# Kernel tuning notes

Measured on AMD Instinct MI355X. Metric: run time of the kernel, lower is better.

Reference implementation:

```python
import jax, jax.numpy as jnp
import numpy as np

N_HEADS = 16


def setup_inputs() -> dict:
    key = jax.random.key(0)
    ks = jax.random.split(key, 5)
    B, S, D = 2, 2048, 1024
    x = jax.random.normal(ks[0], (B, S, D), dtype=jnp.float32)
    Wqkv = jax.random.normal(ks[1], (D, 3 * D), dtype=jnp.float32) * (1.0 / np.sqrt(D))
    bqkv = jax.random.normal(ks[2], (3 * D,), dtype=jnp.float32) * 0.02
    Wout = jax.random.normal(ks[3], (D, D), dtype=jnp.float32) * (1.0 / np.sqrt(D))
    bout = jax.random.normal(ks[4], (D,), dtype=jnp.float32) * 0.02
    return {"x": x, "Wqkv": Wqkv, "bqkv": bqkv, "Wout": Wout, "bout": bout}


def reference(x, Wqkv, bqkv, Wout, bout):
    B, S, D = x.shape
    H = N_HEADS
    dh = D // H
    # qkv projection, then view as [B,S,H,3*dh] and chunk on last dim
    # (matches torch: per-head q/k/v are interleaved slices of the projection)
    qkv = (x @ Wqkv + bqkv).reshape(B, S, H, 3 * dh).transpose(0, 2, 1, 3)  # [B,H,S,3dh]
    q, k, v = jnp.split(qkv, 3, axis=-1)  # each [B,H,S,dh]
    scale = jnp.asarray(1.0 / np.sqrt(dh), dtype=x.dtype)
    scores = jnp.einsum('bhqd,bhkd->bhqk', q, k) * scale  # [B,H,S,S]
    causal = jnp.tril(jnp.ones((S, S), dtype=bool))
    scores = jnp.where(causal, scores, jnp.asarray(-jnp.inf, dtype=scores.dtype))
    attn_w = jax.nn.softmax(scores, axis=-1)
    attn = jnp.einsum('bhqk,bhkd->bhqd', attn_w, v)  # [B,H,S,dh]
    attn = attn.transpose(0, 2, 1, 3).reshape(B, S, D)
    return attn @ Wout + bout
```

## Files before the change

### kernel.cpp

```cpp
#include <hip/hip_runtime.h>
#include <hip/hip_bf16.h>
#include <cstdint>
#include <cstddef>

typedef __hip_bfloat16 bf16;
typedef short bf16x4 __attribute__((ext_vector_type(4)));
typedef short bf16x8 __attribute__((ext_vector_type(8)));
typedef float f32x4 __attribute__((ext_vector_type(4)));

#define LOG2E 1.44269504088896f

static constexpr int Bb = 2, S = 2048, D = 1024, H = 16, DH = 64;

struct TrueT  { static constexpr bool value = true;  };
struct FalseT { static constexpr bool value = false; };

__device__ inline short f2bf_bits(float f) {
  bf16 b = __float2bfloat16(f);
  short s;
  __builtin_memcpy(&s, &b, 2);
  return s;
}
__device__ inline float bfbits2f(short s) {
  uint32_t u = ((uint32_t)(uint16_t)s) << 16;
  float f;
  __builtin_memcpy(&f, &u, 4);
  return f;
}

__global__ __launch_bounds__(256) void prep_kernel(
    const float* __restrict__ Wqkv, bf16* __restrict__ wqkvT,
    const float* __restrict__ Wout, bf16* __restrict__ woutT,
    const float* __restrict__ x, bf16* __restrict__ xbf) {
  const int blk = blockIdx.x;
  const int tid = threadIdx.x;
  if (blk < 4096) {
    __shared__ float t[32][33];
    const float* in;
    bf16* out;
    int R, C, bx, by;
    if (blk < 3072) { in = Wqkv; out = wqkvT; R = 1024; C = 3072; bx = blk % 96; by = blk / 96; }
    else            { in = Wout; out = woutT; R = 1024; C = 1024; bx = (blk - 3072) % 32; by = (blk - 3072) / 32; }
    int c0 = bx * 32, r0 = by * 32;
    int tx = tid & 31, ty = tid >> 5;
#pragma unroll
    for (int i = 0; i < 4; i++) {
      int r = ty + i * 8;
      t[r][tx] = in[(size_t)(r0 + r) * C + c0 + tx];
    }
    __syncthreads();
#pragma unroll
    for (int i = 0; i < 4; i++) {
      int c = ty + i * 8;
      out[(size_t)(c0 + c) * R + r0 + tx] = __float2bfloat16(t[tx][c]);
    }
  } else {
    size_t i = ((size_t)(blk - 4096) * 256 + tid) * 8;
    f32x4 a = *(const f32x4*)(x + i);
    f32x4 b = *(const f32x4*)(x + i + 4);
    bf16x8 v;
#pragma unroll
    for (int j = 0; j < 4; j++) { v[j] = f2bf_bits(a[j]); v[4 + j] = f2bf_bits(b[j]); }
    *(bf16x8*)((short*)xbf + i) = v;
  }
}

__global__ __launch_bounds__(256) void gemm_qkv(
    const bf16* __restrict__ A, const bf16* __restrict__ Bt,
    const float* __restrict__ bias,
    bf16* __restrict__ Qb, bf16* __restrict__ Kb, bf16* __restrict__ Vtb) {
  constexpr int K = 1024;
  __shared__ __align__(16) short smA[128 * 32];
  __shared__ __align__(16) short smB[128 * 32];
  __shared__ __align__(16) short smE[4][16 * 72];

  const int tid = threadIdx.x;
  const int wave = tid >> 6, lane = tid & 63;
  const int quad = lane >> 4, l16 = lane & 15;
  const int m0 = blockIdx.y * 128, n0 = blockIdx.x * 128;
  const int wm = wave >> 1, wn = wave & 1;

  f32x4 acc[4][4];
#pragma unroll
  for (int i = 0; i < 4; i++)
#pragma unroll
    for (int j = 0; j < 4; j++) acc[i][j] = {0.f, 0.f, 0.f, 0.f};

  const int srow = lane >> 2;
  const int scol = (lane & 3) * 8;

  for (int k0 = 0; k0 < K; k0 += 32) {
#pragma unroll
    for (int half = 0; half < 2; half++) {
      int row = half * 64 + wave * 16 + srow;
      const bf16* ga = A + (size_t)(m0 + row) * K + k0 + scol;
      const bf16* gb = Bt + (size_t)(n0 + row) * K + k0 + scol;
      __builtin_amdgcn_global_load_lds(
          (const __attribute__((address_space(1))) void*)ga,
          (__attribute__((address_space(3))) void*)&smA[(half * 64 + wave * 16) * 32],
          16, 0, 0);
      __builtin_amdgcn_global_load_lds(
          (const __attribute__((address_space(1))) void*)gb,
          (__attribute__((address_space(3))) void*)&smB[(half * 64 + wave * 16) * 32],
          16, 0, 0);
    }
    __syncthreads();

    bf16x8 af[4], bf_[4];
#pragma unroll
    for (int mi = 0; mi < 4; mi++)
      af[mi] = *(const bf16x8*)&smA[(wm * 64 + mi * 16 + l16) * 32 + quad * 8];
#pragma unroll
    for (int ni = 0; ni < 4; ni++)
      bf_[ni] = *(const bf16x8*)&smB[(wn * 64 + ni * 16 + l16) * 32 + quad * 8];
#pragma unroll
    for (int mi = 0; mi < 4; mi++)
#pragma unroll
      for (int ni = 0; ni < 4; ni++)
        acc[mi][ni] = __builtin_amdgcn_mfma_f32_16x16x32_bf16(
            af[mi], bf_[ni], acc[mi][ni], 0, 0, 0);
    __syncthreads();
  }

  const int cs0 = n0 + wn * 64;
  const int h = cs0 / 192;
  const int rt = (cs0 >> 6) % 3;
  const int t0w = m0 + wm * 64;
  const int b = t0w >> 11, s0w = t0w & 2047;

  float bv[4];
#pragma unroll
  for (int ni = 0; ni < 4; ni++) bv[ni] = bias[cs0 + ni * 16 + l16];

  if (rt < 2) {
    const float qscale = (rt == 0) ? (0.125f * LOG2E) : 1.0f;
    bf16* dst = (rt == 0 ? Qb : Kb) + ((size_t)(b * H + h) * S + s0w) * 64;
    short* sE = &smE[wave][0];
    const int r8 = lane >> 2, s4 = lane & 3;
#pragma unroll
    for (int mi = 0; mi < 4; mi++) {
#pragma unroll
      for (int ni = 0; ni < 4; ni++)
#pragma unroll
        for (int r = 0; r < 4; r++)
          sE[(quad * 4 + r) * 72 + ni * 16 + l16] =
              f2bf_bits((acc[mi][ni][r] + bv[ni]) * qscale);
      asm volatile("s_waitcnt lgkmcnt(0)" ::: "memory");
      bf16x8 w0 = *(const bf16x8*)&sE[r8 * 72 + s4 * 16];
      bf16x8 w1 = *(const bf16x8*)&sE[r8 * 72 + s4 * 16 + 8];
      short* g = (short*)dst + (size_t)(mi * 16 + r8) * 64 + s4 * 16;
      *(bf16x8*)g = w0;
      *(bf16x8*)(g + 8) = w1;
      asm volatile("s_waitcnt lgkmcnt(0)" ::: "memory");
    }
  } else {
#pragma unroll
    for (int ni = 0; ni < 4; ni++) {
      const int dh = ni * 16 + l16;
#pragma unroll
      for (int mi = 0; mi < 4; mi++) {
        const int s0 = s0w + mi * 16 + quad * 4;
        size_t base = ((size_t)(b * H + h) * 64 + dh) * S + s0;
        bf16x4 vv;
#pragma unroll
        for (int r = 0; r < 4; r++) vv[r] = f2bf_bits(acc[mi][ni][r] + bv[ni]);
        *(bf16x4*)((short*)Vtb + base) = vv;
      }
    }
  }
}

__global__ __launch_bounds__(256) void gemm_out(
    const bf16* __restrict__ A, const bf16* __restrict__ Bt,
    const float* __restrict__ bias, float* __restrict__ C,
    int M, int N, int K) {
  constexpr int BN = 64, NF = 2;
  __shared__ __align__(16) short smA[128 * 32];
  __shared__ __align__(16) short smB[BN * 32];
  __shared__ __align__(16) float smEf[4][580];

  const int tid = threadIdx.x;
  const int wave = tid >> 6, lane = tid & 63;
  const int quad = lane >> 4, l16 = lane & 15;
  const int m0 = blockIdx.y * 128, n0 = blockIdx.x * BN;
  const int wm = wave >> 1, wn = wave & 1;

  f32x4 acc[4][NF];
#pragma unroll
  for (int i = 0; i < 4; i++)
#pragma unroll
    for (int j = 0; j < NF; j++) acc[i][j] = {0.f, 0.f, 0.f, 0.f};

  const int srow = lane >> 2;
  const int scol = (lane & 3) * 8;

  for (int k0 = 0; k0 < K; k0 += 32) {
#pragma unroll
    for (int half = 0; half < 2; half++) {
      int row = half * 64 + wave * 16 + srow;
      const bf16* ga = A + (size_t)(m0 + row) * K + k0 + scol;
      __builtin_amdgcn_global_load_lds(
          (const __attribute__((address_space(1))) void*)ga,
          (__attribute__((address_space(3))) void*)&smA[(half * 64 + wave * 16) * 32],
          16, 0, 0);
    }
    {
      int row = wave * 16 + srow;
      const bf16* gb = Bt + (size_t)(n0 + row) * K + k0 + scol;
      __builtin_amdgcn_global_load_lds(
          (const __attribute__((address_space(1))) void*)gb,
          (__attribute__((address_space(3))) void*)&smB[(wave * 16) * 32],
          16, 0, 0);
    }
    __syncthreads();

    bf16x8 af[4], bf_[NF];
#pragma unroll
    for (int mi = 0; mi < 4; mi++)
      af[mi] = *(const bf16x8*)&smA[(wm * 64 + mi * 16 + l16) * 32 + quad * 8];
#pragma unroll
    for (int ni = 0; ni < NF; ni++)
      bf_[ni] = *(const bf16x8*)&smB[(wn * 32 + ni * 16 + l16) * 32 + quad * 8];
#pragma unroll
    for (int mi = 0; mi < 4; mi++)
#pragma unroll
      for (int ni = 0; ni < NF; ni++)
        acc[mi][ni] = __builtin_amdgcn_mfma_f32_16x16x32_bf16(
            af[mi], bf_[ni], acc[mi][ni], 0, 0, 0);
    __syncthreads();
  }

  float bv[NF];
#pragma unroll
  for (int ni = 0; ni < NF; ni++) bv[ni] = bias[n0 + wn * 32 + ni * 16 + l16];

  float* sE = &smEf[wave][0];
#pragma unroll
  for (int mi = 0; mi < 4; mi++) {
#pragma unroll
    for (int ni = 0; ni < NF; ni++)
#pragma unroll
      for (int r = 0; r < 4; r++)
        sE[(quad * 4 + r) * 36 + ni * 16 + l16] = acc[mi][ni][r] + bv[ni];
    asm volatile("s_waitcnt lgkmcnt(0)" ::: "memory");
#pragma unroll
    for (int t = 0; t < 2; t++) {
      int slot = t * 64 + lane;
      int rr = slot >> 3, c4 = slot & 7;
      f32x4 v = *(const f32x4*)&sE[rr * 36 + c4 * 4];
      int row = m0 + wm * 64 + mi * 16 + rr;
      int col = n0 + wn * 32 + c4 * 4;
      *(f32x4*)&C[(size_t)row * N + col] = v;
    }
    asm volatile("s_waitcnt lgkmcnt(0)" ::: "memory");
  }
}

__global__ __launch_bounds__(256) void attn_kernel(
    const bf16* __restrict__ Qb, const bf16* __restrict__ Kb,
    const bf16* __restrict__ Vtb,
    bf16* __restrict__ Op0, bf16* __restrict__ Op1,
    float* __restrict__ lp0, float* __restrict__ lp1,
    bf16* __restrict__ Ofinal, int split) {
  const int blk = blockIdx.x;
  const int xcd = blk & 7;
  const int idx = blk >> 3;
  int sk, p, bh;
  if (split == 2) { bh = xcd + 8 * (idx / 32); int r = idx % 32; p = r & 15; sk = r >> 4; }
  else            { bh = xcd + 8 * (idx / 16); p = idx & 15; sk = 0; }
  const int h = bh & (H - 1), b = bh >> 4;
  const int tid = threadIdx.x;
  const int wave = tid >> 6, lane = tid & 63;
  const int quad = lane >> 4, l16 = lane & 15;

  bf16*  __restrict__ Op = sk ? Op1 : Op0;
  float* __restrict__ lp = sk ? lp1 : lp0;

  const bf16* Qh = Qb + (size_t)(b * H + h) * S * 64;
  const bf16* Kh = Kb + (size_t)(b * H + h) * S * 64;
  const bf16* Vth = Vtb + (size_t)(b * H + h) * 64 * S;

  __shared__ __align__(16) short smK[2][64 * 64];
  __shared__ __align__(16) short smVt[2][64 * 64];
  __shared__ __align__(16) short pLds[4][16][64];

  const int lrow = lane >> 3;
  const int lg = lane & 7;
  const int swz = l16 & 7;
  const int psw = (l16 & 7) << 1;

  bf16x8 onesB;
#pragma unroll
  for (int j = 0; j < 8; j++) onesB[j] = (short)0x3F80;

  auto stage = [&](int it2, int bufi) {
    const int kv0 = it2 * 64;
#pragma unroll
    for (int j = 0; j < 2; j++) {
      const int row = wave * 16 + j * 8 + lrow;
      const bf16* ks = Kh + (size_t)(kv0 + row) * 64 + (lg ^ (row & 7)) * 8;
      __builtin_amdgcn_global_load_lds(
          (const __attribute__((address_space(1))) void*)ks,
          (__attribute__((address_space(3))) void*)&smK[bufi][(wave * 16 + j * 8) * 64],
          16, 0, 0);
      const bf16* vs = Vth + (size_t)row * S + kv0 + (lg ^ (row & 7)) * 8;
      __builtin_amdgcn_global_load_lds(
          (const __attribute__((address_space(1))) void*)vs,
          (__attribute__((address_space(3))) void*)&smVt[bufi][(wave * 16 + j * 8) * 64],
          16, 0, 0);
    }
  };

#pragma unroll
  for (int pass = 0; pass < 2; pass++) {
    const int qt = pass ? p : (31 - p);
    const int q0 = qt * 64 + wave * 16;
    const int qglob = q0 + l16;

    bf16x8 aQ[2];
#pragma unroll
    for (int kh = 0; kh < 2; kh++)
      aQ[kh] = *(const bf16x8*)(Qh + (size_t)(q0 + l16) * 64 + kh * 32 + quad * 8);

    f32x4 o[4];
#pragma unroll
    for (int dt = 0; dt < 4; dt++) o[dt] = {0.f, 0.f, 0.f, 0.f};
    f32x4 lacc = {0.f, 0.f, 0.f, 0.f};

    auto compute_tile = [&](int it2, int bufi, auto diag_tag) {
      constexpr bool DIAG = decltype(diag_tag)::value;
      const int kv0 = it2 * 64;

      f32x4 z[4];
      __builtin_amdgcn_s_setprio(1);
#pragma unroll
      for (int nh = 0; nh < 4; nh++) {
        const int row = nh * 16 + l16;
        f32x4 t = {0.f, 0.f, 0.f, 0.f};
#pragma unroll
        for (int kh = 0; kh < 2; kh++) {
          bf16x8 bK = *(const bf16x8*)&smK[bufi][row * 64 + ((kh * 4 + quad) ^ swz) * 8];
          t = __builtin_amdgcn_mfma_f32_16x16x32_bf16(bK, aQ[kh], t, 0, 0, 0);
        }
        z[nh] = t;
      }
      __builtin_amdgcn_s_setprio(0);

#pragma unroll
      for (int nh = 0; nh < 4; nh++) {
        bf16x4 pk;
#pragma unroll
        for (int r = 0; r < 4; r++) {
          float e = exp2f(z[nh][r]);
          if (DIAG) {
            const int kidx = kv0 + nh * 16 + quad * 4 + r;
            e = (kidx <= qglob) ? e : 0.f;
          }
          pk[r] = f2bf_bits(e);
        }
        const int gw = (nh * 4 + quad) ^ psw;
        *(bf16x4*)&pLds[wave][l16][gw * 4] = pk;
      }

      asm volatile("s_waitcnt lgkmcnt(0)" ::: "memory");

      bf16x8 aP[2];
#pragma unroll
      for (int k2 = 0; k2 < 2; k2++) {
        const int gr = (k2 * 8 + quad * 2) ^ psw;
        aP[k2] = *(const bf16x8*)&pLds[wave][l16][gr * 4];
      }
      __builtin_amdgcn_s_setprio(1);
#pragma unroll
      for (int k2 = 0; k2 < 2; k2++)
        lacc = __builtin_amdgcn_mfma_f32_16x16x32_bf16(aP[k2], onesB, lacc, 0, 0, 0);
#pragma unroll
      for (int dt = 0; dt < 4; dt++) {
        const int row = dt * 16 + l16;
#pragma unroll
        for (int k2 = 0; k2 < 2; k2++) {
          bf16x8 bV = *(const bf16x8*)&smVt[bufi][row * 64 + ((k2 * 4 + quad) ^ swz) * 8];
          o[dt] = __builtin_amdgcn_mfma_f32_16x16x32_bf16(aP[k2], bV, o[dt], 0, 0, 0);
        }
      }
      __builtin_amdgcn_s_setprio(0);
    };

    int it = sk;
    __syncthreads();
    if (it <= qt) stage(it, 0);
    __syncthreads();
    int cur = 0;
    while (it <= qt) {
      const int next = it + split;
      if (next <= qt) stage(next, cur ^ 1);
      if (it == qt) compute_tile(it, cur, TrueT{});
      else          compute_tile(it, cur, FalseT{});
      __syncthreads();
      cur ^= 1;
      it = next;
    }

    const int rl = lane >> 2, cq = lane & 3;
    short* pw = &pLds[wave][0][0];
    if (split > 1) {
      const size_t rowbase = (size_t)(b * H + h) * S + q0;
      if (l16 == 0) {
#pragma unroll
        for (int r = 0; r < 4; r++) lp[rowbase + quad * 4 + r] = lacc[r];
      }
#pragma unroll
      for (int dt = 0; dt < 4; dt++)
#pragma unroll
        for (int r = 0; r < 4; r++)
          pw[(quad * 4 + r) * 64 + dt * 16 + l16] = f2bf_bits(o[dt][r]);
      asm volatile("s_waitcnt lgkmcnt(0)" ::: "memory");
      bf16x8 w0 = *(const bf16x8*)&pw[rl * 64 + cq * 16];
      bf16x8 w1 = *(const bf16x8*)&pw[rl * 64 + cq * 16 + 8];
      short* g = (short*)Op + (rowbase + rl) * 64 + cq * 16;
      *(bf16x8*)g = w0;
      *(bf16x8*)(g + 8) = w1;
      asm volatile("s_waitcnt lgkmcnt(0)" ::: "memory");
    } else {
      float invr[4];
#pragma unroll
      for (int r = 0; r < 4; r++) invr[r] = 1.f / lacc[r];
#pragma unroll
      for (int dt = 0; dt < 4; dt++)
#pragma unroll
        for (int r = 0; r < 4; r++)
          pw[(quad * 4 + r) * 64 + dt * 16 + l16] = f2bf_bits(o[dt][r] * invr[r]);
      asm volatile("s_waitcnt lgkmcnt(0)" ::: "memory");
      bf16x8 w0 = *(const bf16x8*)&pw[rl * 64 + cq * 16];
      bf16x8 w1 = *(const bf16x8*)&pw[rl * 64 + cq * 16 + 8];
      short* g = (short*)Ofinal + (size_t)(b * S + q0 + rl) * D + h * 64 + cq * 16;
      *(bf16x8*)g = w0;
      *(bf16x8*)(g + 8) = w1;
      asm volatile("s_waitcnt lgkmcnt(0)" ::: "memory");
    }
  }
}

__global__ __launch_bounds__(256) void attn_reduce(
    const bf16* __restrict__ O0, const bf16* __restrict__ O1,
    const float* __restrict__ l0, const float* __restrict__ l1,
    bf16* __restrict__ attnO) {
  int gid = blockIdx.x * 256 + threadIdx.x;
  int row = gid >> 3;
  int c8 = (gid & 7) * 8;
  float inv = 1.f / (l0[row] + l1[row]);
  bf16x8 a = *(const bf16x8*)((const short*)O0 + (size_t)row * 64 + c8);
  bf16x8 bb = *(const bf16x8*)((const short*)O1 + (size_t)row * 64 + c8);
  bf16x8 o;
#pragma unroll
  for (int j = 0; j < 8; j++)
    o[j] = f2bf_bits((bfbits2f(a[j]) + bfbits2f(bb[j])) * inv);
  int bh = row >> 11, q = row & 2047;
  int b = bh >> 4, h = bh & 15;
  *(bf16x8*)((short*)attnO + (((size_t)(b * S + q) * H + h) * 64 + c8)) = o;
}

extern "C" void kernel_launch(void* const* d_in, const int* in_sizes, int n_in,
                              void* d_out, int out_size, void* d_ws, size_t ws_size,
                              hipStream_t stream) {
  const float* x    = (const float*)d_in[0];
  const float* Wqkv = (const float*)d_in[1];
  const float* bqkv = (const float*)d_in[2];
  const float* Wout = (const float*)d_in[3];
  const float* bout = (const float*)d_in[4];
  float* out = (float*)d_out;

  char* ws = (char*)d_ws;
  const bool split2 = (ws_size >= 50855936);

  bf16* Qb  = (bf16*)(ws);
  bf16* Kb  = (bf16*)(ws + 8388608);
  bf16* Vtb = (bf16*)(ws + 16777216);
  bf16* xbf = (bf16*)(ws + 25165824);

  bf16 *Op0 = nullptr, *Op1 = nullptr, *attnO;
  float *lp0 = nullptr, *lp1 = nullptr;
  bf16 *wqkvT, *woutT;
  if (split2) {
    Op0   = (bf16*)(ws + 25165824);
    Op1   = (bf16*)(ws + 33554432);
    lp0   = (float*)(ws + 41943040);
    lp1   = (float*)(ws + 42205184);
    attnO = (bf16*)(ws + 8388608);
    wqkvT = (bf16*)(ws + 42467328);
    woutT = (bf16*)(ws + 48758784);
  } else {
    attnO = (bf16*)(ws + 25165824);
    wqkvT = (bf16*)(ws + 33554432);
    woutT = (bf16*)(ws + 39845888);
  }

  prep_kernel<<<dim3(6144), 256, 0, stream>>>(Wqkv, wqkvT, Wout, woutT, x, xbf);

  gemm_qkv<<<dim3(3072 / 128, 4096 / 128), 256, 0, stream>>>(
      xbf, wqkvT, bqkv, Qb, Kb, Vtb);

  if (split2) {
    attn_kernel<<<dim3(1024), 256, 0, stream>>>(
        Qb, Kb, Vtb, Op0, Op1, lp0, lp1, nullptr, 2);
    attn_reduce<<<dim3(2048), 256, 0, stream>>>(Op0, Op1, lp0, lp1, attnO);
  } else {
    attn_kernel<<<dim3(512), 256, 0, stream>>>(
        Qb, Kb, Vtb, nullptr, nullptr, nullptr, nullptr, attnO, 1);
  }

  gemm_out<<<dim3(1024 / 64, 4096 / 128), 256, 0, stream>>>(
      attnO, woutT, bout, out, 4096, 1024, 1024);
}
```

Measured before the change: 194.7 us.

## Swizzle GEMM LDS tiles, pad attention P buffer, drop split-KV attention path

Both GEMM kernels now XOR-swizzle the 16-byte column chunk on the global-to-LDS load and apply the same swizzle on the MFMA fragment reads, aiming to cut LDS bank conflicts. The attention P/output staging buffer switches from an XOR swizzle to a padded row stride of 76. The two-way KV split and its reduce kernel are removed, so attention always runs 512 blocks and normalizes in place. This saves a kernel launch and the partial-output traffic, but it lowers parallelism for the long causal rows.

Result: faster. 184.1 us (-5.4%).

```diff
diff --git a/kernel.cpp b/kernel.cpp
--- a/kernel.cpp
+++ b/kernel.cpp
@@ -87,7 +87,8 @@
     for (int j = 0; j < 4; j++) acc[i][j] = {0.f, 0.f, 0.f, 0.f};
 
   const int srow = lane >> 2;
-  const int scol = (lane & 3) * 8;
+  const int scol = ((lane & 3) ^ ((lane >> 3) & 3)) * 8;
+  const int gsw = (l16 >> 1) & 3;
 
   for (int k0 = 0; k0 < K; k0 += 32) {
 #pragma unroll
@@ -109,10 +110,10 @@
     bf16x8 af[4], bf_[4];
 #pragma unroll
     for (int mi = 0; mi < 4; mi++)
-      af[mi] = *(const bf16x8*)&smA[(wm * 64 + mi * 16 + l16) * 32 + quad * 8];
+      af[mi] = *(const bf16x8*)&smA[(wm * 64 + mi * 16 + l16) * 32 + (quad ^ gsw) * 8];
 #pragma unroll
     for (int ni = 0; ni < 4; ni++)
-      bf_[ni] = *(const bf16x8*)&smB[(wn * 64 + ni * 16 + l16) * 32 + quad * 8];
+      bf_[ni] = *(const bf16x8*)&smB[(wn * 64 + ni * 16 + l16) * 32 + (quad ^ gsw) * 8];
 #pragma unroll
     for (int mi = 0; mi < 4; mi++)
 #pragma unroll
@@ -192,7 +193,8 @@
     for (int j = 0; j < NF; j++) acc[i][j] = {0.f, 0.f, 0.f, 0.f};
 
   const int srow = lane >> 2;
-  const int scol = (lane & 3) * 8;
+  const int scol = ((lane & 3) ^ ((lane >> 3) & 3)) * 8;
+  const int gsw = (l16 >> 1) & 3;
 
   for (int k0 = 0; k0 < K; k0 += 32) {
 #pragma unroll
@@ -217,10 +219,10 @@
     bf16x8 af[4], bf_[NF];
 #pragma unroll
     for (int mi = 0; mi < 4; mi++)
-      af[mi] = *(const bf16x8*)&smA[(wm * 64 + mi * 16 + l16) * 32 + quad * 8];
+      af[mi] = *(const bf16x8*)&smA[(wm * 64 + mi * 16 + l16) * 32 + (quad ^ gsw) * 8];
 #pragma unroll
     for (int ni = 0; ni < NF; ni++)
-      bf_[ni] = *(const bf16x8*)&smB[(wn * 32 + ni * 16 + l16) * 32 + quad * 8];
+      bf_[ni] = *(const bf16x8*)&smB[(wn * 32 + ni * 16 + l16) * 32 + (quad ^ gsw) * 8];
 #pragma unroll
     for (int mi = 0; mi < 4; mi++)
 #pragma unroll
@@ -258,36 +260,28 @@
 
 __global__ __launch_bounds__(256) void attn_kernel(
     const bf16* __restrict__ Qb, const bf16* __restrict__ Kb,
-    const bf16* __restrict__ Vtb,
-    bf16* __restrict__ Op0, bf16* __restrict__ Op1,
-    float* __restrict__ lp0, float* __restrict__ lp1,
-    bf16* __restrict__ Ofinal, int split) {
+    const bf16* __restrict__ Vtb, bf16* __restrict__ Ofinal) {
   const int blk = blockIdx.x;
   const int xcd = blk & 7;
   const int idx = blk >> 3;
-  int sk, p, bh;
-  if (split == 2) { bh = xcd + 8 * (idx / 32); int r = idx % 32; p = r & 15; sk = r >> 4; }
-  else            { bh = xcd + 8 * (idx / 16); p = idx & 15; sk = 0; }
+  const int bh = xcd + 8 * (idx >> 4);
+  const int p = idx & 15;
   const int h = bh & (H - 1), b = bh >> 4;
   const int tid = threadIdx.x;
   const int wave = tid >> 6, lane = tid & 63;
   const int quad = lane >> 4, l16 = lane & 15;
 
-  bf16*  __restrict__ Op = sk ? Op1 : Op0;
-  float* __restrict__ lp = sk ? lp1 : lp0;
-
   const bf16* Qh = Qb + (size_t)(b * H + h) * S * 64;
   const bf16* Kh = Kb + (size_t)(b * H + h) * S * 64;
   const bf16* Vth = Vtb + (size_t)(b * H + h) * 64 * S;
 
   __shared__ __align__(16) short smK[2][64 * 64];
   __shared__ __align__(16) short smVt[2][64 * 64];
-  __shared__ __align__(16) short pLds[4][16][64];
+  __shared__ __align__(16) short pLds[4][16][76];
 
   const int lrow = lane >> 3;
   const int lg = lane & 7;
   const int swz = l16 & 7;
-  const int psw = (l16 & 7) << 1;
 
   bf16x8 onesB;
 #pragma unroll
@@ -358,18 +352,15 @@
           }
           pk[r] = f2bf_bits(e);
         }
-        const int gw = (nh * 4 + quad) ^ psw;
-        *(bf16x4*)&pLds[wave][l16][gw * 4] = pk;
+        *(bf16x4*)&pLds[wave][l16][nh * 16 + quad * 4] = pk;
       }
 
       asm volatile("s_waitcnt lgkmcnt(0)" ::: "memory");
 
       bf16x8 aP[2];
 #pragma unroll
-      for (int k2 = 0; k2 < 2; k2++) {
-        const int gr = (k2 * 8 + quad * 2) ^ psw;
-        aP[k2] = *(const bf16x8*)&pLds[wave][l16][gr * 4];
-      }
+      for (int k2 = 0; k2 < 2; k2++)
+        aP[k2] = *(const bf16x8*)&pLds[wave][l16][k2 * 32 + quad * 8];
       __builtin_amdgcn_s_setprio(1);
 #pragma unroll
       for (int k2 = 0; k2 < 2; k2++)
@@ -386,13 +377,13 @@
       __builtin_amdgcn_s_setprio(0);
     };
 
-    int it = sk;
-    __syncthreads();
-    if (it <= qt) stage(it, 0);
+    int it = 0;
+    __syncthreads();
+    stage(it, 0);
     __syncthreads();
     int cur = 0;
     while (it <= qt) {
-      const int next = it + split;
+      const int next = it + 1;
       if (next <= qt) stage(next, cur ^ 1);
       if (it == qt) compute_tile(it, cur, TrueT{});
       else          compute_tile(it, cur, FalseT{});
@@ -401,63 +392,26 @@
       it = next;
     }
 
-    const int rl = lane >> 2, cq = lane & 3;
+    float inv[4];
+#pragma unroll
+    for (int r = 0; r < 4; r++) inv[r] = 1.f / lacc[r];
     short* pw = &pLds[wave][0][0];
-    if (split > 1) {
-      const size_t rowbase = (size_t)(b * H + h) * S + q0;
-      if (l16 == 0) {
-#pragma unroll
-        for (int r = 0; r < 4; r++) lp[rowbase + quad * 4 + r] = lacc[r];
-      }
-#pragma unroll
-      for (int dt = 0; dt < 4; dt++)
-#pragma unroll
-        for (int r = 0; r < 4; r++)
-          pw[(quad * 4 + r) * 64 + dt * 16 + l16] = f2bf_bits(o[dt][r]);
-      asm volatile("s_waitcnt lgkmcnt(0)" ::: "memory");
-      bf16x8 w0 = *(const bf16x8*)&pw[rl * 64 + cq * 16];
-      bf16x8 w1 = *(const bf16x8*)&pw[rl * 64 + cq * 16 + 8];
-      short* g = (short*)Op + (rowbase + rl) * 64 + cq * 16;
-      *(bf16x8*)g = w0;
-      *(bf16x8*)(g + 8) = w1;
-      asm volatile("s_waitcnt lgkmcnt(0)" ::: "memory");
-    } else {
-      float invr[4];
-#pragma unroll
-      for (int r = 0; r < 4; r++) invr[r] = 1.f / lacc[r];
-#pragma unroll
-      for (int dt = 0; dt < 4; dt++)
-#pragma unroll
-        for (int r = 0; r < 4; r++)
-          pw[(quad * 4 + r) * 64 + dt * 16 + l16] = f2bf_bits(o[dt][r] * invr[r]);
-      asm volatile("s_waitcnt lgkmcnt(0)" ::: "memory");
-      bf16x8 w0 = *(const bf16x8*)&pw[rl * 64 + cq * 16];
-      bf16x8 w1 = *(const bf16x8*)&pw[rl * 64 + cq * 16 + 8];
+#pragma unroll
+    for (int dt = 0; dt < 4; dt++)
+#pragma unroll
+      for (int r = 0; r < 4; r++)
+        pw[(quad * 4 + r) * 76 + dt * 16 + l16] = f2bf_bits(o[dt][r] * inv[r]);
+    asm volatile("s_waitcnt lgkmcnt(0)" ::: "memory");
+    {
+      const int rl = lane >> 2, cq = lane & 3;
+      bf16x8 w0 = *(const bf16x8*)&pw[rl * 76 + cq * 16];
+      bf16x8 w1 = *(const bf16x8*)&pw[rl * 76 + cq * 16 + 8];
       short* g = (short*)Ofinal + (size_t)(b * S + q0 + rl) * D + h * 64 + cq * 16;
       *(bf16x8*)g = w0;
       *(bf16x8*)(g + 8) = w1;
-      asm volatile("s_waitcnt lgkmcnt(0)" ::: "memory");
-    }
-  }
-}
-
-__global__ __launch_bounds__(256) void attn_reduce(
-    const bf16* __restrict__ O0, const bf16* __restrict__ O1,
-    const float* __restrict__ l0, const float* __restrict__ l1,
-    bf16* __restrict__ attnO) {
-  int gid = blockIdx.x * 256 + threadIdx.x;
-  int row = gid >> 3;
-  int c8 = (gid & 7) * 8;
-  float inv = 1.f / (l0[row] + l1[row]);
-  bf16x8 a = *(const bf16x8*)((const short*)O0 + (size_t)row * 64 + c8);
-  bf16x8 bb = *(const bf16x8*)((const short*)O1 + (size_t)row * 64 + c8);
-  bf16x8 o;
-#pragma unroll
-  for (int j = 0; j < 8; j++)
-    o[j] = f2bf_bits((bfbits2f(a[j]) + bfbits2f(bb[j])) * inv);
-  int bh = row >> 11, q = row & 2047;
-  int b = bh >> 4, h = bh & 15;
-  *(bf16x8*)((short*)attnO + (((size_t)(b * S + q) * H + h) * 64 + c8)) = o;
+    }
+    asm volatile("s_waitcnt lgkmcnt(0)" ::: "memory");
+  }
 }
 
 extern "C" void kernel_launch(void* const* d_in, const int* in_sizes, int n_in,
@@ -471,43 +425,21 @@
   float* out = (float*)d_out;
 
   char* ws = (char*)d_ws;
-  const bool split2 = (ws_size >= 50855936);
-
-  bf16* Qb  = (bf16*)(ws);
-  bf16* Kb  = (bf16*)(ws + 8388608);
-  bf16* Vtb = (bf16*)(ws + 16777216);
-  bf16* xbf = (bf16*)(ws + 25165824);
-
-  bf16 *Op0 = nullptr, *Op1 = nullptr, *attnO;
-  float *lp0 = nullptr, *lp1 = nullptr;
-  bf16 *wqkvT, *woutT;
-  if (split2) {
-    Op0   = (bf16*)(ws + 25165824);
-    Op1   = (bf16*)(ws + 33554432);
-    lp0   = (float*)(ws + 41943040);
-    lp1   = (float*)(ws + 42205184);
-    attnO = (bf16*)(ws + 8388608);
-    wqkvT = (bf16*)(ws + 42467328);
-    woutT = (bf16*)(ws + 48758784);
-  } else {
-    attnO = (bf16*)(ws + 25165824);
-    wqkvT = (bf16*)(ws + 33554432);
-    woutT = (bf16*)(ws + 39845888);
-  }
+
+  bf16* Qb    = (bf16*)(ws);
+  bf16* Kb    = (bf16*)(ws + 8388608);
+  bf16* Vtb   = (bf16*)(ws + 16777216);
+  bf16* xbf   = (bf16*)(ws + 25165824);
+  bf16* attnO = (bf16*)(ws + 25165824);
+  bf16* wqkvT = (bf16*)(ws + 33554432);
+  bf16* woutT = (bf16*)(ws + 39845888);
 
   prep_kernel<<<dim3(6144), 256, 0, stream>>>(Wqkv, wqkvT, Wout, woutT, x, xbf);
 
   gemm_qkv<<<dim3(3072 / 128, 4096 / 128), 256, 0, stream>>>(
       xbf, wqkvT, bqkv, Qb, Kb, Vtb);
 
-  if (split2) {
-    attn_kernel<<<dim3(1024), 256, 0, stream>>>(
-        Qb, Kb, Vtb, Op0, Op1, lp0, lp1, nullptr, 2);
-    attn_reduce<<<dim3(2048), 256, 0, stream>>>(Op0, Op1, lp0, lp1, attnO);
-  } else {
-    attn_kernel<<<dim3(512), 256, 0, stream>>>(
-        Qb, Kb, Vtb, nullptr, nullptr, nullptr, nullptr, attnO, 1);
-  }
+  attn_kernel<<<dim3(512), 256, 0, stream>>>(Qb, Kb, Vtb, attnO);
 
   gemm_out<<<dim3(1024 / 64, 4096 / 128), 256, 0, stream>>>(
       attnO, woutT, bout, out, 4096, 1024, 1024);
```

## Swizzle GEMM LDS tiles, load V directly from global, pad P scratch

Applied to the files above, without the earlier changes.

Both GEMM kernels now XOR-swizzle the 8-element column groups in their LDS A/B tiles, so fragment reads avoid bank conflicts. The attention kernel stops staging V^T through LDS and has each wave read its V fragments straight from global memory inside the tile compute. The P scratch buffer drops its XOR swizzle in favour of a padded row stride of 76. This saves LDS space and staging traffic, but V loads are no longer prefetched and now sit on the critical path, duplicated across the four waves.

Measured after the change: 235.3 us. 1.21x slower.

```diff
diff --git a/kernel.cpp b/kernel.cpp
--- a/kernel.cpp
+++ b/kernel.cpp
@@ -87,7 +87,8 @@
     for (int j = 0; j < 4; j++) acc[i][j] = {0.f, 0.f, 0.f, 0.f};
 
   const int srow = lane >> 2;
-  const int scol = (lane & 3) * 8;
+  const int scol = ((lane & 3) ^ ((lane >> 3) & 3)) * 8;
+  const int gsw = (l16 >> 1) & 3;
 
   for (int k0 = 0; k0 < K; k0 += 32) {
 #pragma unroll
@@ -109,10 +110,10 @@
     bf16x8 af[4], bf_[4];
 #pragma unroll
     for (int mi = 0; mi < 4; mi++)
-      af[mi] = *(const bf16x8*)&smA[(wm * 64 + mi * 16 + l16) * 32 + quad * 8];
+      af[mi] = *(const bf16x8*)&smA[(wm * 64 + mi * 16 + l16) * 32 + (quad ^ gsw) * 8];
 #pragma unroll
     for (int ni = 0; ni < 4; ni++)
-      bf_[ni] = *(const bf16x8*)&smB[(wn * 64 + ni * 16 + l16) * 32 + quad * 8];
+      bf_[ni] = *(const bf16x8*)&smB[(wn * 64 + ni * 16 + l16) * 32 + (quad ^ gsw) * 8];
 #pragma unroll
     for (int mi = 0; mi < 4; mi++)
 #pragma unroll
@@ -192,7 +193,8 @@
     for (int j = 0; j < NF; j++) acc[i][j] = {0.f, 0.f, 0.f, 0.f};
 
   const int srow = lane >> 2;
-  const int scol = (lane & 3) * 8;
+  const int scol = ((lane & 3) ^ ((lane >> 3) & 3)) * 8;
+  const int gsw = (l16 >> 1) & 3;
 
   for (int k0 = 0; k0 < K; k0 += 32) {
 #pragma unroll
@@ -217,10 +219,10 @@
     bf16x8 af[4], bf_[NF];
 #pragma unroll
     for (int mi = 0; mi < 4; mi++)
-      af[mi] = *(const bf16x8*)&smA[(wm * 64 + mi * 16 + l16) * 32 + quad * 8];
+      af[mi] = *(const bf16x8*)&smA[(wm * 64 + mi * 16 + l16) * 32 + (quad ^ gsw) * 8];
 #pragma unroll
     for (int ni = 0; ni < NF; ni++)
-      bf_[ni] = *(const bf16x8*)&smB[(wn * 32 + ni * 16 + l16) * 32 + quad * 8];
+      bf_[ni] = *(const bf16x8*)&smB[(wn * 32 + ni * 16 + l16) * 32 + (quad ^ gsw) * 8];
 #pragma unroll
     for (int mi = 0; mi < 4; mi++)
 #pragma unroll
@@ -281,13 +283,11 @@
   const bf16* Vth = Vtb + (size_t)(b * H + h) * 64 * S;
 
   __shared__ __align__(16) short smK[2][64 * 64];
-  __shared__ __align__(16) short smVt[2][64 * 64];
-  __shared__ __align__(16) short pLds[4][16][64];
+  __shared__ __align__(16) short pLds[4][16][76];
 
   const int lrow = lane >> 3;
   const int lg = lane & 7;
   const int swz = l16 & 7;
-  const int psw = (l16 & 7) << 1;
 
   bf16x8 onesB;
 #pragma unroll
@@ -303,11 +303,6 @@
           (const __attribute__((address_space(1))) void*)ks,
           (__attribute__((address_space(3))) void*)&smK[bufi][(wave * 16 + j * 8) * 64],
           16, 0, 0);
-      const bf16* vs = Vth + (size_t)row * S + kv0 + (lg ^ (row & 7)) * 8;
-      __builtin_amdgcn_global_load_lds(
-          (const __attribute__((address_space(1))) void*)vs,
-          (__attribute__((address_space(3))) void*)&smVt[bufi][(wave * 16 + j * 8) * 64],
-          16, 0, 0);
     }
   };
 
@@ -330,6 +325,14 @@
     auto compute_tile = [&](int it2, int bufi, auto diag_tag) {
       constexpr bool DIAG = decltype(diag_tag)::value;
       const int kv0 = it2 * 64;
+
+      bf16x8 vf[4][2];
+#pragma unroll
+      for (int dt = 0; dt < 4; dt++)
+#pragma unroll
+        for (int k2 = 0; k2 < 2; k2++)
+          vf[dt][k2] = *(const bf16x8*)(
+              Vth + (size_t)(dt * 16 + l16) * S + kv0 + (k2 * 4 + quad) * 8);
 
       f32x4 z[4];
       __builtin_amdgcn_s_setprio(1);
@@ -358,31 +361,24 @@
           }
           pk[r] = f2bf_bits(e);
         }
-        const int gw = (nh * 4 + quad) ^ psw;
-        *(bf16x4*)&pLds[wave][l16][gw * 4] = pk;
+        *(bf16x4*)&pLds[wave][l16][nh * 16 + quad * 4] = pk;
       }
 
       asm volatile("s_waitcnt lgkmcnt(0)" ::: "memory");
 
       bf16x8 aP[2];
 #pragma unroll
-      for (int k2 = 0; k2 < 2; k2++) {
-        const int gr = (k2 * 8 + quad * 2) ^ psw;
-        aP[k2] = *(const bf16x8*)&pLds[wave][l16][gr * 4];
-      }
+      for (int k2 = 0; k2 < 2; k2++)
+        aP[k2] = *(const bf16x8*)&pLds[wave][l16][k2 * 32 + quad * 8];
       __builtin_amdgcn_s_setprio(1);
 #pragma unroll
       for (int k2 = 0; k2 < 2; k2++)
         lacc = __builtin_amdgcn_mfma_f32_16x16x32_bf16(aP[k2], onesB, lacc, 0, 0, 0);
 #pragma unroll
-      for (int dt = 0; dt < 4; dt++) {
-        const int row = dt * 16 + l16;
-#pragma unroll
-        for (int k2 = 0; k2 < 2; k2++) {
-          bf16x8 bV = *(const bf16x8*)&smVt[bufi][row * 64 + ((k2 * 4 + quad) ^ swz) * 8];
-          o[dt] = __builtin_amdgcn_mfma_f32_16x16x32_bf16(aP[k2], bV, o[dt], 0, 0, 0);
-        }
-      }
+      for (int dt = 0; dt < 4; dt++)
+#pragma unroll
+        for (int k2 = 0; k2 < 2; k2++)
+          o[dt] = __builtin_amdgcn_mfma_f32_16x16x32_bf16(aP[k2], vf[dt][k2], o[dt], 0, 0, 0);
       __builtin_amdgcn_s_setprio(0);
     };
 
@@ -401,7 +397,6 @@
       it = next;
     }
 
-    const int rl = lane >> 2, cq = lane & 3;
     short* pw = &pLds[wave][0][0];
     if (split > 1) {
       const size_t rowbase = (size_t)(b * H + h) * S + q0;
@@ -413,29 +408,35 @@
       for (int dt = 0; dt < 4; dt++)
 #pragma unroll
         for (int r = 0; r < 4; r++)
-          pw[(quad * 4 + r) * 64 + dt * 16 + l16] = f2bf_bits(o[dt][r]);
-      asm volatile("s_waitcnt lgkmcnt(0)" ::: "memory");
-      bf16x8 w0 = *(const bf16x8*)&pw[rl * 64 + cq * 16];
-      bf16x8 w1 = *(const bf16x8*)&pw[rl * 64 + cq * 16 + 8];
-      short* g = (short*)Op + (rowbase + rl) * 64 + cq * 16;
-      *(bf16x8*)g = w0;
-      *(bf16x8*)(g + 8) = w1;
+          pw[(quad * 4 + r) * 76 + dt * 16 + l16] = f2bf_bits(o[dt][r]);
+      asm volatile("s_waitcnt lgkmcnt(0)" ::: "memory");
+      {
+        const int rl = lane >> 2, cq = lane & 3;
+        bf16x8 w0 = *(const bf16x8*)&pw[rl * 76 + cq * 16];
+        bf16x8 w1 = *(const bf16x8*)&pw[rl * 76 + cq * 16 + 8];
+        short* g = (short*)Op + (rowbase + rl) * 64 + cq * 16;
+        *(bf16x8*)g = w0;
+        *(bf16x8*)(g + 8) = w1;
+      }
       asm volatile("s_waitcnt lgkmcnt(0)" ::: "memory");
     } else {
-      float invr[4];
-#pragma unroll
-      for (int r = 0; r < 4; r++) invr[r] = 1.f / lacc[r];
+      float inv[4];
+#pragma unroll
+      for (int r = 0; r < 4; r++) inv[r] = 1.f / lacc[r];
 #pragma unroll
       for (int dt = 0; dt < 4; dt++)
 #pragma unroll
         for (int r = 0; r < 4; r++)
-          pw[(quad * 4 + r) * 64 + dt * 16 + l16] = f2bf_bits(o[dt][r] * invr[r]);
-      asm volatile("s_waitcnt lgkmcnt(0)" ::: "memory");
-      bf16x8 w0 = *(const bf16x8*)&pw[rl * 64 + cq * 16];
-      bf16x8 w1 = *(const bf16x8*)&pw[rl * 64 + cq * 16 + 8];
-      short* g = (short*)Ofinal + (size_t)(b * S + q0 + rl) * D + h * 64 + cq * 16;
-      *(bf16x8*)g = w0;
-      *(bf16x8*)(g + 8) = w1;
+          pw[(quad * 4 + r) * 76 + dt * 16 + l16] = f2bf_bits(o[dt][r] * inv[r]);
+      asm volatile("s_waitcnt lgkmcnt(0)" ::: "memory");
+      {
+        const int rl = lane >> 2, cq = lane & 3;
+        bf16x8 w0 = *(const bf16x8*)&pw[rl * 76 + cq * 16];
+        bf16x8 w1 = *(const bf16x8*)&pw[rl * 76 + cq * 16 + 8];
+        short* g = (short*)Ofinal + (size_t)(b * S + q0 + rl) * D + h * 64 + cq * 16;
+        *(bf16x8*)g = w0;
+        *(bf16x8*)(g + 8) = w1;
+      }
       asm volatile("s_waitcnt lgkmcnt(0)" ::: "memory");
     }
   }
```
